# Optimization experiments

Hardware: AMD Instinct MI355X
Metric: run time of the kernel (lower is better)

Reference implementation:

```python
import jax, jax.numpy as jnp
import numpy as np

B, D, G, C = 4096, 512, 128, 10
THR = 0.95          # reliability_threshold
LR_MAX, LR_MIN = 0.2, 0.05
CTX_MAX, CTX_MIN = 2, 0


def setup_inputs() -> dict:
    key = jax.random.key(0)
    k1, k2, k3, k4, k5 = jax.random.split(key, 5)
    activations = jax.random.uniform(k1, (B, D), jnp.float32)
    labels = jax.random.randint(k2, (B,), 0, C)
    som_vectors = jax.random.uniform(k3, (G, G, D), jnp.float32) * 0.5 + 0.5
    cell_labels = jax.random.randint(k4, (G, G), 0, C)
    cell_reliability = jax.random.uniform(k5, (G, G), jnp.float32) * 100.0
    return dict(activations=activations, labels=labels, som_vectors=som_vectors,
                cell_labels=cell_labels, cell_reliability=cell_reliability,
                epoch=10, max_epochs=100)


def reference(activations, labels, som_vectors, cell_labels, cell_reliability, epoch, max_epochs):
    # --- schedule (static python scalars) ---
    progress = (max_epochs - epoch) / max_epochs if max_epochs > 0 else 0
    progress = max(0.0, min(1.0, progress))
    som_context = CTX_MIN + int(progress ** 4 * (CTX_MAX - CTX_MIN))
    som_lr = LR_MIN + progress * (LR_MAX - LR_MIN)

    flat_som = som_vectors.reshape(-1, D)                 # (N, D), N = G*G
    # --- squared-euclidean distance matrix (B, N) ---
    x_norm = jnp.sum(activations ** 2, axis=1, keepdims=True)
    w_norm = jnp.sum(flat_som ** 2, axis=1)[None, :]
    dists = jnp.clip(x_norm + w_norm - 2.0 * activations @ flat_som.T, 0.0, None)
    min_dists = jnp.min(dists, axis=1)
    bmu = jnp.argmin(dists, axis=1)                        # (B,)

    # --- class-constrained BMU for SOM error ---
    flat_labels = cell_labels.reshape(-1)
    label_mask = flat_labels[None, :] != labels[:, None]   # (B, N)
    class_dists = jnp.where(label_mask, jnp.inf, dists)
    class_bmu = jnp.argmin(class_dists, axis=1)
    class_bmu_vectors = flat_som[class_bmu]                # (B, D)
    rel = cell_reliability.reshape(-1)[class_bmu] / 100.0  # (B,)
    valid = (rel >= THR).astype(activations.dtype)
    som_errors = 0.01 * rel[:, None] * (class_bmu_vectors - activations) * valid[:, None]

    # --- batch neighborhood SOM update (matches torch code, incl. x/y convention) ---
    bmu_x = bmu // G
    bmu_y = bmu % G
    coords = jnp.arange(G)
    dist_y = jnp.abs(coords[None, :] - bmu_y[:, None])     # (B, G) rows (y_grid) vs bmu_y
    dist_x = jnp.abs(coords[None, :] - bmu_x[:, None])     # (B, G) cols (x_grid) vs bmu_x
    cheb = jnp.maximum(dist_y[:, :, None], dist_x[:, None, :])   # (B, G, G)
    powers = (som_lr / 2.0 ** cheb.astype(activations.dtype)) * (cheb <= som_context)
    denom = powers.sum(axis=0)[..., None]                  # (G, G, 1)
    numerator = jnp.einsum('bn,bd->nd', powers.reshape(B, -1), activations).reshape(G, G, D)
    updated = som_vectors + numerator - som_vectors * denom
    new_som = jnp.where(jnp.mean(min_dists) > 1e-4, updated, som_vectors)

    return som_errors, new_som
```

## Files before the change

### kernel.cpp

```cpp
#include <hip/hip_runtime.h>
#include <math.h>

#define B_ 4096
#define D_ 512
#define G_ 128
#define N_ (G_*G_)
#define NTP 64
#define THR_ 0.95f
#define IMAX_ 0x7FFFFFFF

typedef float f32x4 __attribute__((ext_vector_type(4)));
typedef _Float16 half8 __attribute__((ext_vector_type(8)));

__global__ __launch_bounds__(256) void prep_kernel(
    const float* __restrict__ A, const float* __restrict__ W,
    _Float16* __restrict__ Ahi, _Float16* __restrict__ Whi,
    float* __restrict__ wnorm, float* __restrict__ S,
    float* __restrict__ count, float* __restrict__ sum_min)
{
    const int blk = blockIdx.x, tid = threadIdx.x;
    if (blk < 2048) {
        int i = blk * 256 + tid;
        float4 v = ((const float4*)A)[i];
        float vv[4] = {v.x, v.y, v.z, v.w};
        union { _Float16 h[4]; uint64_t u64; } H;
        #pragma unroll
        for (int j = 0; j < 4; j++) H.h[j] = (_Float16)vv[j];
        ((uint64_t*)Ahi)[i] = H.u64;
    } else if (blk < 6144) {
        int n = (blk - 2048) * 4 + (tid >> 6);
        int t = tid & 63;
        const float* row = W + (size_t)n * D_;
        float4 a = ((const float4*)row)[t];
        float4 b = ((const float4*)row)[t + 64];
        float av[4] = {a.x, a.y, a.z, a.w}, bv[4] = {b.x, b.y, b.z, b.w};
        union { _Float16 h[4]; uint64_t u64; } Ha, Hb;
        #pragma unroll
        for (int j = 0; j < 4; j++) { Ha.h[j] = (_Float16)av[j]; Hb.h[j] = (_Float16)bv[j]; }
        ((uint64_t*)(Whi + (size_t)n * D_))[t]       = Ha.u64;
        ((uint64_t*)(Whi + (size_t)n * D_ + 256))[t] = Hb.u64;
        float s = a.x*a.x + a.y*a.y + a.z*a.z + a.w*a.w
                + b.x*b.x + b.y*b.y + b.z*b.z + b.w*b.w;
        #pragma unroll
        for (int off = 32; off > 0; off >>= 1) s += __shfl_down(s, off, 64);
        if (t == 0) wnorm[n] = s;
    } else if (blk < 6160) {
        if (blk == 6144 && tid < 65) sum_min[tid] = 0.f;
        int j = (blk - 6144) * 256 + tid;
        float4 z = {0.f, 0.f, 0.f, 0.f};
        ((float4*)count)[j] = z;
    } else {
        size_t i = (size_t)(blk - 6160) * 256 + tid;
        float4 z = {0.f, 0.f, 0.f, 0.f};
        ((float4*)S)[i] = z;
    }
}

__device__ __forceinline__ unsigned long long packmin(float v, int n) {
    unsigned u = __float_as_uint(v);
    u ^= (u & 0x80000000u) ? 0xFFFFFFFFu : 0x80000000u;
    return ((unsigned long long)u << 32) | (unsigned)n;
}
__device__ __forceinline__ void unpackmin(unsigned long long pkt, float* v, int* n) {
    unsigned u = (unsigned)(pkt >> 32);
    u = (u & 0x80000000u) ? (u ^ 0x80000000u) : ~u;
    *v = __uint_as_float(u);
    *n = (int)(unsigned)pkt;
}


#define PH_WAIT_(N) asm volatile("s_waitcnt vmcnt(" #N ")" ::: "memory")
#define PH_WAIT(N) PH_WAIT_(N)
#define WAITLGKM0 asm volatile("s_waitcnt lgkmcnt(0)" ::: "memory")
#define SBAR __builtin_amdgcn_s_barrier()
#define SCHED0 __builtin_amdgcn_sched_barrier(0)
#define PRIO1 __builtin_amdgcn_s_setprio(1)
#define PRIO0 __builtin_amdgcn_s_setprio(0)

#define STAGE_HALF(GBASE, LOFF, TAU, H) do { \
    __builtin_amdgcn_global_load_lds( \
        (const __attribute__((address_space(1))) void*)((GBASE) + (size_t)(H) * (128 * D_) + (TAU) * 64 + srcoff0), \
        (__attribute__((address_space(3))) void*)(smem + (LOFF) + (((TAU) & 1) << 15) + ((H) << 14) + ldsoff0), 16, 0, 0); \
    __builtin_amdgcn_global_load_lds( \
        (const __attribute__((address_space(1))) void*)((GBASE) + (size_t)(H) * (128 * D_) + (TAU) * 64 + srcoff1), \
        (__attribute__((address_space(3))) void*)(smem + (LOFF) + (((TAU) & 1) << 15) + ((H) << 14) + ldsoff1), 16, 0, 0); \
} while (0)

#define TILE(TAU, S1, S3, S4, DO_W, VM4) do { \
    half8 af[4][2], bl[2][2], bh[2][2]; \
    _Pragma("unroll") for (int mi = 0; mi < 4; mi++) { \
        af[mi][0] = *(const half8*)(smem + (((TAU) & 1) << 15) + sA + mi * 2048 + swz0); \
        af[mi][1] = *(const half8*)(smem + (((TAU) & 1) << 15) + sA + mi * 2048 + swz1); } \
    _Pragma("unroll") for (int ni = 0; ni < 2; ni++) { \
        bl[ni][0] = *(const half8*)(smem + 65536 + (((TAU) & 1) << 15) + sB + ni * 2048 + swz0); \
        bl[ni][1] = *(const half8*)(smem + 65536 + (((TAU) & 1) << 15) + sB + ni * 2048 + swz1); } \
    if (S1) STAGE_HALF(Abase, 0, (TAU) + 1, 1); \
    SBAR; WAITLGKM0; SCHED0; PRIO1; \
    _Pragma("unroll") for (int mi = 0; mi < 4; mi++) \
      _Pragma("unroll") for (int ni = 0; ni < 2; ni++) { \
        acc[mi][ni] = __builtin_amdgcn_mfma_f32_16x16x32_f16(af[mi][0], bl[ni][0], acc[mi][ni], 0, 0, 0); \
        acc[mi][ni] = __builtin_amdgcn_mfma_f32_16x16x32_f16(af[mi][1], bl[ni][1], acc[mi][ni], 0, 0, 0); } \
    PRIO0; SCHED0; SBAR; \
    _Pragma("unroll") for (int ni = 0; ni < 2; ni++) { \
        bh[ni][0] = *(const half8*)(smem + 65536 + (((TAU) & 1) << 15) + sB + (ni + 2) * 2048 + swz0); \
        bh[ni][1] = *(const half8*)(smem + 65536 + (((TAU) & 1) << 15) + sB + (ni + 2) * 2048 + swz1); } \
    SBAR; WAITLGKM0; SCHED0; PRIO1; \
    _Pragma("unroll") for (int mi = 0; mi < 4; mi++) \
      _Pragma("unroll") for (int ni = 0; ni < 2; ni++) { \
        acc[mi][ni + 2] = __builtin_amdgcn_mfma_f32_16x16x32_f16(af[mi][0], bh[ni][0], acc[mi][ni + 2], 0, 0, 0); \
        acc[mi][ni + 2] = __builtin_amdgcn_mfma_f32_16x16x32_f16(af[mi][1], bh[ni][1], acc[mi][ni + 2], 0, 0, 0); } \
    PRIO0; SCHED0; SBAR; \
    _Pragma("unroll") for (int mi = 0; mi < 4; mi++) { \
        af[mi][0] = *(const half8*)(smem + (((TAU) & 1) << 15) + sA + (mi + 4) * 2048 + swz0); \
        af[mi][1] = *(const half8*)(smem + (((TAU) & 1) << 15) + sA + (mi + 4) * 2048 + swz1); } \
    if (S3) STAGE_HALF(Wbase, 65536, (TAU) + 2, 0); \
    SBAR; WAITLGKM0; SCHED0; PRIO1; \
    _Pragma("unroll") for (int mi = 0; mi < 4; mi++) \
      _Pragma("unroll") for (int ni = 0; ni < 2; ni++) { \
        acc[mi + 4][ni + 2] = __builtin_amdgcn_mfma_f32_16x16x32_f16(af[mi][0], bh[ni][0], acc[mi + 4][ni + 2], 0, 0, 0); \
        acc[mi + 4][ni + 2] = __builtin_amdgcn_mfma_f32_16x16x32_f16(af[mi][1], bh[ni][1], acc[mi + 4][ni + 2], 0, 0, 0); } \
    PRIO0; SCHED0; SBAR; \
    if (S4) { STAGE_HALF(Abase, 0, (TAU) + 2, 0); STAGE_HALF(Wbase, 65536, (TAU) + 2, 1); } \
    if (DO_W) PH_WAIT(VM4); \
    SBAR; PRIO1; \
    _Pragma("unroll") for (int mi = 0; mi < 4; mi++) \
      _Pragma("unroll") for (int ni = 0; ni < 2; ni++) { \
        acc[mi + 4][ni] = __builtin_amdgcn_mfma_f32_16x16x32_f16(af[mi][0], bl[ni][0], acc[mi + 4][ni], 0, 0, 0); \
        acc[mi + 4][ni] = __builtin_amdgcn_mfma_f32_16x16x32_f16(af[mi][1], bl[ni][1], acc[mi + 4][ni], 0, 0, 0); } \
    PRIO0; SCHED0; SBAR; \
} while (0)

__global__ __launch_bounds__(512, 2) void score_mfma_kernel(
    const _Float16* __restrict__ Ah, const _Float16* __restrict__ Wh,
    const float* __restrict__ wnorm,
    const int* __restrict__ labels, const int* __restrict__ clabels,
    float* __restrict__ pminv, int* __restrict__ pmini,
    float* __restrict__ pcminv, int* __restrict__ pcmini)
{
    __shared__ __align__(16) char smem[131072];

    const int tid  = threadIdx.x;
    const int lane = tid & 63;
    const int wave = tid >> 6;
    const int wm = wave >> 2, wn = wave & 3;
    const int c = lane & 15, quad = lane >> 4;

    const int o = blockIdx.x;
    const int xcd = o & 7, idx = o >> 3;
    const int ntile = (xcd << 3) | (idx & 7);
    const int mtile = idx >> 3;
    const int m0 = mtile * 256, n0 = ntile * 256;

    const _Float16* Abase = Ah + (size_t)m0 * D_;
    const _Float16* Wbase = Wh + (size_t)n0 * D_;

    const int i0 = tid, i1 = 512 + tid;
    const int rl0 = i0 >> 3, sl0 = i0 & 7, rl1 = i1 >> 3, sl1 = i1 & 7;
    const size_t srcoff0 = (size_t)rl0 * D_ + ((sl0 ^ (rl0 & 7)) << 3);
    const size_t srcoff1 = (size_t)rl1 * D_ + ((sl1 ^ (rl1 & 7)) << 3);
    const int ldsoff0 = i0 << 4, ldsoff1 = i1 << 4;

    const int sA = (wm * 128 + c) * 128;
    const int sB = (wn * 64 + c) * 128;
    const int swz0 = ((0 * 4 + quad) ^ (c & 7)) << 4;
    const int swz1 = ((1 * 4 + quad) ^ (c & 7)) << 4;

    f32x4 acc[8][4];
    #pragma unroll
    for (int i = 0; i < 8; i++)
        #pragma unroll
        for (int j = 0; j < 4; j++)
            acc[i][j] = (f32x4){0.f, 0.f, 0.f, 0.f};

    STAGE_HALF(Abase, 0, 0, 0);
    STAGE_HALF(Wbase, 65536, 0, 0);
    STAGE_HALF(Wbase, 65536, 0, 1);
    STAGE_HALF(Abase, 0, 0, 1);
    STAGE_HALF(Abase, 0, 1, 0);
    STAGE_HALF(Wbase, 65536, 1, 0);
    STAGE_HALF(Wbase, 65536, 1, 1);
    PH_WAIT(6); SBAR;

    TILE(0, 1, 1, 1, 1, 6);
    TILE(1, 1, 1, 1, 1, 6);
    TILE(2, 1, 1, 1, 1, 6);
    TILE(3, 1, 1, 1, 1, 6);
    TILE(4, 1, 1, 1, 1, 6);
    TILE(5, 1, 1, 1, 1, 6);
    TILE(6, 1, 0, 0, 1, 0);
    TILE(7, 0, 0, 0, 0, 0);

    __syncthreads();

    const unsigned long long ID = (0xFF800000ull << 32) | 0x7FFFFFFFull;
    float wnl[4]; int cll[4];
    #pragma unroll
    for (int ni = 0; ni < 4; ni++) {
        int n = n0 + wn * 64 + ni * 16 + c;
        wnl[ni] = wnorm[n];
        cll[ni] = clabels[n];
    }

    unsigned long long (*tbl)[64] = (unsigned long long (*)[64])smem;
    unsigned long long cbst[8][4];

    #pragma unroll
    for (int mi = 0; mi < 8; mi++) {
        #pragma unroll
        for (int r = 0; r < 4; r++) {
            int rowl = wm * 128 + mi * 16 + quad * 4 + r;
            int lb = labels[m0 + rowl];
            unsigned long long bb = ID, cb = ID;
            #pragma unroll
            for (int ni = 0; ni < 4; ni++) {
                float s = fmaf(-2.f, acc[mi][ni][r], wnl[ni]);
                unsigned long long pk = packmin(s, n0 + wn * 64 + ni * 16 + c);
                bb = bb < pk ? bb : pk;
                if (cll[ni] == lb) cb = cb < pk ? cb : pk;
            }
            tbl[rowl][(wn * 16 + c) ^ (rowl & 15)] = bb;
            cbst[mi][r] = cb;
        }
    }
    __syncthreads();
    if (tid < 256) {
        int row = tid;
        unsigned long long m = ID;
        #pragma unroll
        for (int j = 0; j < 64; j++) {
            unsigned long long v = tbl[row][j ^ (row & 15)];
            m = m < v ? m : v;
        }
        float v; int n; unpackmin(m, &v, &n);
        size_t pp = (size_t)(m0 + row) * NTP + ntile;
        pminv[pp] = v; pmini[pp] = n;
    }
    __syncthreads();
    #pragma unroll
    for (int mi = 0; mi < 8; mi++)
        #pragma unroll
        for (int r = 0; r < 4; r++) {
            int rowl = wm * 128 + mi * 16 + quad * 4 + r;
            tbl[rowl][(wn * 16 + c) ^ (rowl & 15)] = cbst[mi][r];
        }
    __syncthreads();
    if (tid < 256) {
        int row = tid;
        unsigned long long m = ID;
        #pragma unroll
        for (int j = 0; j < 64; j++) {
            unsigned long long v = tbl[row][j ^ (row & 15)];
            m = m < v ? m : v;
        }
        float v; int n; unpackmin(m, &v, &n);
        size_t pp = (size_t)(m0 + row) * NTP + ntile;
        pcminv[pp] = v; pcmini[pp] = n;
    }
}

__global__ __launch_bounds__(256) void reduce_kernel(
    const float* __restrict__ A, const float* __restrict__ W,
    const float* __restrict__ crel,
    const float* __restrict__ pminv, const int* __restrict__ pmini,
    const float* __restrict__ pcminv, const int* __restrict__ pcmini,
    int* __restrict__ bmu, float* __restrict__ sum_min, float* __restrict__ out0,
    float* __restrict__ S, float* __restrict__ count)
{
    __shared__ int sbn[4];
    const int b = blockIdx.x * 4 + (threadIdx.x >> 6);
    const int l = threadIdx.x & 63;

    size_t p = (size_t)b * NTP + l;
    unsigned long long bb = packmin(pminv[p], pmini[p]);
    unsigned long long cb = packmin(pcminv[p], pcmini[p]);

    const float* arow = A + (size_t)b * D_;
    float4 xa = ((const float4*)arow)[l];
    float4 xb = ((const float4*)arow)[l + 64];
    float xs = xa.x*xa.x + xa.y*xa.y + xa.z*xa.z + xa.w*xa.w
             + xb.x*xb.x + xb.y*xb.y + xb.z*xb.z + xb.w*xb.w;

    #pragma unroll
    for (int off = 1; off < 64; off <<= 1) {
        unsigned long long ob = __shfl_xor(bb, off, 64);
        bb = bb < ob ? bb : ob;
        unsigned long long oc = __shfl_xor(cb, off, 64);
        cb = cb < oc ? cb : oc;
        xs += __shfl_xor(xs, off, 64);
    }

    float bv; int bn; unpackmin(bb, &bv, &bn);
    float cv; int cn; unpackmin(cb, &cv, &cn);

    if (l == 0) {
        bmu[b] = bn;
        sbn[threadIdx.x >> 6] = bn;
        float md = xs + bv;
        if (md < 0.f) md = 0.f;
        atomicAdd(&sum_min[b & 63], md);
        atomicAdd(&count[bn], 1.0f);
    }

    float r = crel[cn] / 100.0f;
    float sc = (r >= THR_) ? 0.01f * r : 0.f;
    const float* wrow = W + (size_t)cn * D_;
    float4 wa = ((const float4*)wrow)[l];
    float4 wb = ((const float4*)wrow)[l + 64];
    float4 oa, ob4;
    oa.x = sc * (wa.x - xa.x); oa.y = sc * (wa.y - xa.y);
    oa.z = sc * (wa.z - xa.z); oa.w = sc * (wa.w - xa.w);
    ob4.x = sc * (wb.x - xb.x); ob4.y = sc * (wb.y - xb.y);
    ob4.z = sc * (wb.z - xb.z); ob4.w = sc * (wb.w - xb.w);
    float* orow = out0 + (size_t)b * D_;
    ((float4*)orow)[l]      = oa;
    ((float4*)orow)[l + 64] = ob4;

    __syncthreads();
    const int base_b = blockIdx.x * 4;
    #pragma unroll
    for (int rr = 0; rr < 4; rr++) {
        int bm = sbn[rr];
        const float* ar = A + (size_t)(base_b + rr) * D_;
        float* Sr = S + (size_t)bm * D_;
        atomicAdd(&Sr[threadIdx.x],       ar[threadIdx.x]);
        atomicAdd(&Sr[threadIdx.x + 256], ar[threadIdx.x + 256]);
    }
}

__global__ __launch_bounds__(256) void final_kernel(
    const float* __restrict__ som, const float* __restrict__ S,
    const float* __restrict__ count, const float* __restrict__ sum_min,
    const int* __restrict__ epoch_p, const int* __restrict__ maxep_p,
    float* __restrict__ out1)
{
    __shared__ float gsum;
    if (threadIdx.x == 0) {
        float s = 0.f;
        for (int i = 0; i < 64; i++) s += sum_min[i];
        gsum = s;
    }
    __syncthreads();

    const int o = blockIdx.x;
    const int vb = ((o & 7) << 10) | (o >> 3);
    size_t i4 = (size_t)vb * 256 + threadIdx.x;
    int n = (int)(i4 >> 7);
    int d4 = (int)(i4 & 127);
    float4 s = ((const float4*)som)[i4];
    bool gate = gsum > 1e-4f * (float)B_;
    float4 ov = s;
    if (gate) {
        int ep = epoch_p[0], me = maxep_p[0];
        float progress = (me > 0) ? (float)(me - ep) / (float)me : 0.f;
        progress = fminf(fmaxf(progress, 0.f), 1.f);
        float p2 = progress * progress;
        int ctx = (int)(p2 * p2 * 2.0f);
        float lr = 0.05f + progress * 0.15f;

        int i = n / G_, j = n % G_;
        float4 nu = {0.f, 0.f, 0.f, 0.f};
        float dn = 0.f;
        for (int di = -ctx; di <= ctx; di++) {
            int ia = i - di; if (ia < 0 || ia >= G_) continue;
            for (int dj = -ctx; dj <= ctx; dj++) {
                int jb = j - dj; if (jb < 0 || jb >= G_) continue;
                int ad = abs(di), aj = abs(dj);
                int cheb = ad > aj ? ad : aj;
                float coef = ldexpf(lr, -cheb);
                float4 t4 = ((const float4*)S)[(size_t)(jb * G_ + ia) * 128 + d4];
                nu.x += coef * t4.x; nu.y += coef * t4.y;
                nu.z += coef * t4.z; nu.w += coef * t4.w;
                dn += coef * count[jb * G_ + ia];
            }
        }
        ov.x = s.x + nu.x - s.x * dn;
        ov.y = s.y + nu.y - s.y * dn;
        ov.z = s.z + nu.z - s.z * dn;
        ov.w = s.w + nu.w - s.w * dn;
    }
    ((float4*)out1)[i4] = ov;
}

extern "C" void kernel_launch(void* const* d_in, const int* in_sizes, int n_in,
                              void* d_out, int out_size, void* d_ws, size_t ws_size,
                              hipStream_t stream) {
    const float* A   = (const float*)d_in[0];
    const int*   lab = (const int*)d_in[1];
    const float* W   = (const float*)d_in[2];
    const int*   cl  = (const int*)d_in[3];
    const float* cr  = (const float*)d_in[4];
    const int*   ep  = (const int*)d_in[5];
    const int*   me  = (const int*)d_in[6];

    float* out0 = (float*)d_out;
    float* out1 = out0 + (size_t)B_ * D_;

    const size_t MB = 1024 * 1024;
    uint8_t* w = (uint8_t*)d_ws;
    _Float16* Ahi  = (_Float16*)(w);
    _Float16* Whi  = (_Float16*)(w + 4 * MB);
    float* pminv   = (float*)(w + 32 * MB);
    int*   pmini   = (int*)  (w + 34 * MB);
    float* pcminv  = (float*)(w + 36 * MB);
    int*   pcmini  = (int*)  (w + 38 * MB);
    float* wnorm   = (float*)(w + 40 * MB);
    float* count   = (float*)(w + 40 * MB + 128 * 1024);
    int*   bmu     = (int*)  (w + 40 * MB + 192 * 1024);
    float* sum_min = (float*)(w + 40 * MB + 256 * 1024);

    const int fused = (ws_size >= 80 * MB) ? 1 : 0;
    float* S = fused ? (float*)(w + 48 * MB) : (float*)w;

    prep_kernel<<<fused ? 14352 : 6160, 256, 0, stream>>>(
        A, W, Ahi, Whi, wnorm, S, count, sum_min);

    score_mfma_kernel<<<dim3((B_ / 256) * (N_ / 256)), 512, 0, stream>>>(
        Ahi, Whi, wnorm, lab, cl, pminv, pmini, pcminv, pcmini);

    if (!fused)
        hipMemsetAsync(S, 0, (size_t)N_ * D_ * sizeof(float), stream);

    reduce_kernel<<<B_ / 4, 256, 0, stream>>>(A, W, cr, pminv, pmini, pcminv, pcmini,
                                              bmu, sum_min, out0, S, count);

    final_kernel<<<(N_ * D_ / 4) / 256, 256, 0, stream>>>(
        W, S, count, sum_min, ep, me, out1);
}
```

Measured before the change: 258.1 us.

## Restructure MFMA k-tile pipeline to load all fragments once and stage per tile

Replaces the four-phase per-k-tile schedule, which interleaved partial LDS fragment loads, staged global loads and many barriers, with a simpler schedule. Each tile now loads all A and B fragments up front, runs half the MFMAs, then issues all staging loads for tile+2 and waits before running the other half. The aim is fewer barriers and less LDS/MFMA serialisation. In exchange it holds more fragment registers live and overlaps less finely, which could hurt occupancy or latency hiding at 2 blocks per CU.

Measured after the change: 260.9 us. About the same (+1.1%).

```diff
diff --git a/kernel.cpp b/kernel.cpp
--- a/kernel.cpp
+++ b/kernel.cpp
@@ -86,48 +86,37 @@
         (__attribute__((address_space(3))) void*)(smem + (LOFF) + (((TAU) & 1) << 15) + ((H) << 14) + ldsoff1), 16, 0, 0); \
 } while (0)
 
-#define TILE(TAU, S1, S3, S4, DO_W, VM4) do { \
-    half8 af[4][2], bl[2][2], bh[2][2]; \
-    _Pragma("unroll") for (int mi = 0; mi < 4; mi++) { \
-        af[mi][0] = *(const half8*)(smem + (((TAU) & 1) << 15) + sA + mi * 2048 + swz0); \
-        af[mi][1] = *(const half8*)(smem + (((TAU) & 1) << 15) + sA + mi * 2048 + swz1); } \
-    _Pragma("unroll") for (int ni = 0; ni < 2; ni++) { \
-        bl[ni][0] = *(const half8*)(smem + 65536 + (((TAU) & 1) << 15) + sB + ni * 2048 + swz0); \
-        bl[ni][1] = *(const half8*)(smem + 65536 + (((TAU) & 1) << 15) + sB + ni * 2048 + swz1); } \
-    if (S1) STAGE_HALF(Abase, 0, (TAU) + 1, 1); \
-    SBAR; WAITLGKM0; SCHED0; PRIO1; \
+#define TILE9(TAU, DO_STAGE, VMN, LAST) do { \
+    const int bo_ = ((TAU) & 1) << 15; \
+    half8 af[8][2], bf[4][2]; \
+    _Pragma("unroll") for (int mi = 0; mi < 8; mi++) { \
+        af[mi][0] = *(const half8*)(smem + bo_ + sA + mi * 2048 + swz0); \
+        af[mi][1] = *(const half8*)(smem + bo_ + sA + mi * 2048 + swz1); } \
+    _Pragma("unroll") for (int ni = 0; ni < 4; ni++) { \
+        bf[ni][0] = *(const half8*)(smem + 65536 + bo_ + sB + ni * 2048 + swz0); \
+        bf[ni][1] = *(const half8*)(smem + 65536 + bo_ + sB + ni * 2048 + swz1); } \
+    PRIO1; \
     _Pragma("unroll") for (int mi = 0; mi < 4; mi++) \
-      _Pragma("unroll") for (int ni = 0; ni < 2; ni++) { \
-        acc[mi][ni] = __builtin_amdgcn_mfma_f32_16x16x32_f16(af[mi][0], bl[ni][0], acc[mi][ni], 0, 0, 0); \
-        acc[mi][ni] = __builtin_amdgcn_mfma_f32_16x16x32_f16(af[mi][1], bl[ni][1], acc[mi][ni], 0, 0, 0); } \
-    PRIO0; SCHED0; SBAR; \
-    _Pragma("unroll") for (int ni = 0; ni < 2; ni++) { \
-        bh[ni][0] = *(const half8*)(smem + 65536 + (((TAU) & 1) << 15) + sB + (ni + 2) * 2048 + swz0); \
-        bh[ni][1] = *(const half8*)(smem + 65536 + (((TAU) & 1) << 15) + sB + (ni + 2) * 2048 + swz1); } \
-    SBAR; WAITLGKM0; SCHED0; PRIO1; \
-    _Pragma("unroll") for (int mi = 0; mi < 4; mi++) \
-      _Pragma("unroll") for (int ni = 0; ni < 2; ni++) { \
-        acc[mi][ni + 2] = __builtin_amdgcn_mfma_f32_16x16x32_f16(af[mi][0], bh[ni][0], acc[mi][ni + 2], 0, 0, 0); \
-        acc[mi][ni + 2] = __builtin_amdgcn_mfma_f32_16x16x32_f16(af[mi][1], bh[ni][1], acc[mi][ni + 2], 0, 0, 0); } \
-    PRIO0; SCHED0; SBAR; \
-    _Pragma("unroll") for (int mi = 0; mi < 4; mi++) { \
-        af[mi][0] = *(const half8*)(smem + (((TAU) & 1) << 15) + sA + (mi + 4) * 2048 + swz0); \
-        af[mi][1] = *(const half8*)(smem + (((TAU) & 1) << 15) + sA + (mi + 4) * 2048 + swz1); } \
-    if (S3) STAGE_HALF(Wbase, 65536, (TAU) + 2, 0); \
-    SBAR; WAITLGKM0; SCHED0; PRIO1; \
-    _Pragma("unroll") for (int mi = 0; mi < 4; mi++) \
-      _Pragma("unroll") for (int ni = 0; ni < 2; ni++) { \
-        acc[mi + 4][ni + 2] = __builtin_amdgcn_mfma_f32_16x16x32_f16(af[mi][0], bh[ni][0], acc[mi + 4][ni + 2], 0, 0, 0); \
-        acc[mi + 4][ni + 2] = __builtin_amdgcn_mfma_f32_16x16x32_f16(af[mi][1], bh[ni][1], acc[mi + 4][ni + 2], 0, 0, 0); } \
-    PRIO0; SCHED0; SBAR; \
-    if (S4) { STAGE_HALF(Abase, 0, (TAU) + 2, 0); STAGE_HALF(Wbase, 65536, (TAU) + 2, 1); } \
-    if (DO_W) PH_WAIT(VM4); \
-    SBAR; PRIO1; \
-    _Pragma("unroll") for (int mi = 0; mi < 4; mi++) \
-      _Pragma("unroll") for (int ni = 0; ni < 2; ni++) { \
-        acc[mi + 4][ni] = __builtin_amdgcn_mfma_f32_16x16x32_f16(af[mi][0], bl[ni][0], acc[mi + 4][ni], 0, 0, 0); \
-        acc[mi + 4][ni] = __builtin_amdgcn_mfma_f32_16x16x32_f16(af[mi][1], bl[ni][1], acc[mi + 4][ni], 0, 0, 0); } \
-    PRIO0; SCHED0; SBAR; \
+      _Pragma("unroll") for (int ni = 0; ni < 4; ni++) { \
+        acc[mi][ni] = __builtin_amdgcn_mfma_f32_16x16x32_f16(af[mi][0], bf[ni][0], acc[mi][ni], 0, 0, 0); \
+        acc[mi][ni] = __builtin_amdgcn_mfma_f32_16x16x32_f16(af[mi][1], bf[ni][1], acc[mi][ni], 0, 0, 0); } \
+    PRIO0; \
+    if (!(LAST)) { \
+        WAITLGKM0; SCHED0; SBAR; \
+        if (DO_STAGE) { \
+            STAGE_HALF(Abase, 0, (TAU) + 2, 0); \
+            STAGE_HALF(Abase, 0, (TAU) + 2, 1); \
+            STAGE_HALF(Wbase, 65536, (TAU) + 2, 0); \
+            STAGE_HALF(Wbase, 65536, (TAU) + 2, 1); \
+        } \
+        PH_WAIT(VMN); SBAR; \
+    } \
+    PRIO1; \
+    _Pragma("unroll") for (int mi = 4; mi < 8; mi++) \
+      _Pragma("unroll") for (int ni = 0; ni < 4; ni++) { \
+        acc[mi][ni] = __builtin_amdgcn_mfma_f32_16x16x32_f16(af[mi][0], bf[ni][0], acc[mi][ni], 0, 0, 0); \
+        acc[mi][ni] = __builtin_amdgcn_mfma_f32_16x16x32_f16(af[mi][1], bf[ni][1], acc[mi][ni], 0, 0, 0); } \
+    PRIO0; SCHED0; \
 } while (0)
 
 __global__ __launch_bounds__(512, 2) void score_mfma_kernel(
@@ -173,22 +162,23 @@
             acc[i][j] = (f32x4){0.f, 0.f, 0.f, 0.f};
 
     STAGE_HALF(Abase, 0, 0, 0);
+    STAGE_HALF(Abase, 0, 0, 1);
     STAGE_HALF(Wbase, 65536, 0, 0);
     STAGE_HALF(Wbase, 65536, 0, 1);
-    STAGE_HALF(Abase, 0, 0, 1);
     STAGE_HALF(Abase, 0, 1, 0);
+    STAGE_HALF(Abase, 0, 1, 1);
     STAGE_HALF(Wbase, 65536, 1, 0);
     STAGE_HALF(Wbase, 65536, 1, 1);
-    PH_WAIT(6); SBAR;
-
-    TILE(0, 1, 1, 1, 1, 6);
-    TILE(1, 1, 1, 1, 1, 6);
-    TILE(2, 1, 1, 1, 1, 6);
-    TILE(3, 1, 1, 1, 1, 6);
-    TILE(4, 1, 1, 1, 1, 6);
-    TILE(5, 1, 1, 1, 1, 6);
-    TILE(6, 1, 0, 0, 1, 0);
-    TILE(7, 0, 0, 0, 0, 0);
+    PH_WAIT(8); SBAR;
+
+    TILE9(0, 1, 8, 0);
+    TILE9(1, 1, 8, 0);
+    TILE9(2, 1, 8, 0);
+    TILE9(3, 1, 8, 0);
+    TILE9(4, 1, 8, 0);
+    TILE9(5, 1, 8, 0);
+    TILE9(6, 0, 0, 0);
+    TILE9(7, 0, 0, 1);
 
     __syncthreads();
 
```

## Fuse prep, score, reduce and update kernels into one cooperative persistent kernel

Applied to the files above, without the earlier changes.

Replaces the four-kernel pipeline with a single cooperative kernel of 256 blocks that runs the fp16 conversion, the MFMA score tiles, the BMU reduction and the SOM update as phases separated by grid-wide syncs. The goal is to remove kernel launch gaps and tail effects between stages. In exchange, the score phase now loops over 1024 tiles with only 256 resident blocks, and each phase is limited to the persistent grid's parallelism. Grid syncs add their own overhead, and the fallback path is kept for devices without cooperative launch.

Result: slower. 527.9 us (+104.5%).

```diff
diff --git a/kernel.cpp b/kernel.cpp
--- a/kernel.cpp
+++ b/kernel.cpp
@@ -1,5 +1,8 @@
 #include <hip/hip_runtime.h>
+#include <hip/hip_cooperative_groups.h>
 #include <math.h>
+
+namespace cg = cooperative_groups;
 
 #define B_ 4096
 #define D_ 512
@@ -11,50 +14,6 @@
 
 typedef float f32x4 __attribute__((ext_vector_type(4)));
 typedef _Float16 half8 __attribute__((ext_vector_type(8)));
-
-__global__ __launch_bounds__(256) void prep_kernel(
-    const float* __restrict__ A, const float* __restrict__ W,
-    _Float16* __restrict__ Ahi, _Float16* __restrict__ Whi,
-    float* __restrict__ wnorm, float* __restrict__ S,
-    float* __restrict__ count, float* __restrict__ sum_min)
-{
-    const int blk = blockIdx.x, tid = threadIdx.x;
-    if (blk < 2048) {
-        int i = blk * 256 + tid;
-        float4 v = ((const float4*)A)[i];
-        float vv[4] = {v.x, v.y, v.z, v.w};
-        union { _Float16 h[4]; uint64_t u64; } H;
-        #pragma unroll
-        for (int j = 0; j < 4; j++) H.h[j] = (_Float16)vv[j];
-        ((uint64_t*)Ahi)[i] = H.u64;
-    } else if (blk < 6144) {
-        int n = (blk - 2048) * 4 + (tid >> 6);
-        int t = tid & 63;
-        const float* row = W + (size_t)n * D_;
-        float4 a = ((const float4*)row)[t];
-        float4 b = ((const float4*)row)[t + 64];
-        float av[4] = {a.x, a.y, a.z, a.w}, bv[4] = {b.x, b.y, b.z, b.w};
-        union { _Float16 h[4]; uint64_t u64; } Ha, Hb;
-        #pragma unroll
-        for (int j = 0; j < 4; j++) { Ha.h[j] = (_Float16)av[j]; Hb.h[j] = (_Float16)bv[j]; }
-        ((uint64_t*)(Whi + (size_t)n * D_))[t]       = Ha.u64;
-        ((uint64_t*)(Whi + (size_t)n * D_ + 256))[t] = Hb.u64;
-        float s = a.x*a.x + a.y*a.y + a.z*a.z + a.w*a.w
-                + b.x*b.x + b.y*b.y + b.z*b.z + b.w*b.w;
-        #pragma unroll
-        for (int off = 32; off > 0; off >>= 1) s += __shfl_down(s, off, 64);
-        if (t == 0) wnorm[n] = s;
-    } else if (blk < 6160) {
-        if (blk == 6144 && tid < 65) sum_min[tid] = 0.f;
-        int j = (blk - 6144) * 256 + tid;
-        float4 z = {0.f, 0.f, 0.f, 0.f};
-        ((float4*)count)[j] = z;
-    } else {
-        size_t i = (size_t)(blk - 6160) * 256 + tid;
-        float4 z = {0.f, 0.f, 0.f, 0.f};
-        ((float4*)S)[i] = z;
-    }
-}
 
 __device__ __forceinline__ unsigned long long packmin(float v, int n) {
     unsigned u = __float_as_uint(v);
@@ -130,8 +89,8 @@
     PRIO0; SCHED0; SBAR; \
 } while (0)
 
-__global__ __launch_bounds__(512, 2) void score_mfma_kernel(
-    const _Float16* __restrict__ Ah, const _Float16* __restrict__ Wh,
+__device__ __forceinline__ void score_tile_body(
+    int o, const _Float16* __restrict__ Ah, const _Float16* __restrict__ Wh,
     const float* __restrict__ wnorm,
     const int* __restrict__ labels, const int* __restrict__ clabels,
     float* __restrict__ pminv, int* __restrict__ pmini,
@@ -145,7 +104,6 @@
     const int wm = wave >> 2, wn = wave & 3;
     const int c = lane & 15, quad = lane >> 4;
 
-    const int o = blockIdx.x;
     const int xcd = o & 7, idx = o >> 3;
     const int ntile = (xcd << 3) | (idx & 7);
     const int mtile = idx >> 3;
@@ -256,6 +214,247 @@
         size_t pp = (size_t)(m0 + row) * NTP + ntile;
         pcminv[pp] = v; pcmini[pp] = n;
     }
+    __syncthreads();
+}
+
+__global__ __launch_bounds__(512, 2) void mega_kernel(
+    const float* __restrict__ A, const int* __restrict__ labels,
+    const float* __restrict__ W, const int* __restrict__ clabels,
+    const float* __restrict__ crel,
+    const int* __restrict__ epoch_p, const int* __restrict__ maxep_p,
+    _Float16* __restrict__ Ahi, _Float16* __restrict__ Whi,
+    float* __restrict__ wnorm,
+    float* __restrict__ pminv, int* __restrict__ pmini,
+    float* __restrict__ pcminv, int* __restrict__ pcmini,
+    int* __restrict__ bmu, float* __restrict__ sum_min,
+    float* __restrict__ out0, float* __restrict__ out1,
+    float* __restrict__ S, float* __restrict__ count, int fusedS)
+{
+    cg::grid_group grid = cg::this_grid();
+    const int tid  = threadIdx.x;
+    const int blk  = blockIdx.x;
+    const int gtid = blk * 512 + tid;
+    const int GS   = 256 * 512;
+
+    {
+        const float4 z = {0.f, 0.f, 0.f, 0.f};
+        #pragma unroll
+        for (int it = 0; it < 4; it++) {
+            int i = gtid + it * GS;
+            float4 v = ((const float4*)A)[i];
+            float vv[4] = {v.x, v.y, v.z, v.w};
+            union { _Float16 h[4]; uint64_t u64; } H;
+            #pragma unroll
+            for (int j = 0; j < 4; j++) H.h[j] = (_Float16)vv[j];
+            ((uint64_t*)Ahi)[i] = H.u64;
+        }
+        const int t = tid & 63;
+        #pragma unroll
+        for (int it = 0; it < 8; it++) {
+            int n = (gtid >> 6) + it * (GS >> 6);
+            const float* row = W + (size_t)n * D_;
+            float4 a = ((const float4*)row)[t];
+            float4 bq = ((const float4*)row)[t + 64];
+            float av[4] = {a.x, a.y, a.z, a.w}, bv[4] = {bq.x, bq.y, bq.z, bq.w};
+            union { _Float16 h[4]; uint64_t u64; } Ha, Hb;
+            #pragma unroll
+            for (int j = 0; j < 4; j++) { Ha.h[j] = (_Float16)av[j]; Hb.h[j] = (_Float16)bv[j]; }
+            ((uint64_t*)(Whi + (size_t)n * D_))[t]       = Ha.u64;
+            ((uint64_t*)(Whi + (size_t)n * D_ + 256))[t] = Hb.u64;
+            float s = a.x*a.x + a.y*a.y + a.z*a.z + a.w*a.w
+                    + bq.x*bq.x + bq.y*bq.y + bq.z*bq.z + bq.w*bq.w;
+            #pragma unroll
+            for (int off = 32; off > 0; off >>= 1) s += __shfl_down(s, off, 64);
+            if (t == 0) wnorm[n] = s;
+        }
+        if (gtid < N_ / 4) ((float4*)count)[gtid] = z;
+        if (gtid < 65) sum_min[gtid] = 0.f;
+        if (fusedS) {
+            #pragma unroll
+            for (int it = 0; it < 16; it++)
+                ((float4*)S)[(size_t)gtid + (size_t)it * GS] = z;
+        }
+    }
+    __threadfence();
+    grid.sync();
+
+    for (int o = blk; o < 1024; o += 256)
+        score_tile_body(o, Ahi, Whi, wnorm, labels, clabels,
+                        pminv, pmini, pcminv, pcmini);
+    __threadfence();
+    grid.sync();
+
+    if (!fusedS) {
+        const float4 z = {0.f, 0.f, 0.f, 0.f};
+        #pragma unroll
+        for (int it = 0; it < 16; it++)
+            ((float4*)S)[(size_t)gtid + (size_t)it * GS] = z;
+        __threadfence();
+        grid.sync();
+    }
+
+    {
+        const int l = tid & 63;
+        #pragma unroll
+        for (int it = 0; it < 2; it++) {
+            int rw = (gtid >> 6) + it * (GS >> 6);
+            size_t p = (size_t)rw * NTP + l;
+            unsigned long long bb = packmin(pminv[p], pmini[p]);
+            unsigned long long cb = packmin(pcminv[p], pcmini[p]);
+
+            const float* arow = A + (size_t)rw * D_;
+            float4 xa = ((const float4*)arow)[l];
+            float4 xb = ((const float4*)arow)[l + 64];
+            float xs = xa.x*xa.x + xa.y*xa.y + xa.z*xa.z + xa.w*xa.w
+                     + xb.x*xb.x + xb.y*xb.y + xb.z*xb.z + xb.w*xb.w;
+
+            #pragma unroll
+            for (int off = 1; off < 64; off <<= 1) {
+                unsigned long long ob = __shfl_xor(bb, off, 64);
+                bb = bb < ob ? bb : ob;
+                unsigned long long oc = __shfl_xor(cb, off, 64);
+                cb = cb < oc ? cb : oc;
+                xs += __shfl_xor(xs, off, 64);
+            }
+
+            float bv; int bn; unpackmin(bb, &bv, &bn);
+            float cv; int cn; unpackmin(cb, &cv, &cn);
+
+            if (l == 0) {
+                bmu[rw] = bn;
+                float md = xs + bv;
+                if (md < 0.f) md = 0.f;
+                atomicAdd(&sum_min[rw & 63], md);
+                atomicAdd(&count[bn], 1.0f);
+            }
+
+            float rel = crel[cn] / 100.0f;
+            float sc = (rel >= THR_) ? 0.01f * rel : 0.f;
+            const float* wrow = W + (size_t)cn * D_;
+            float4 wa = ((const float4*)wrow)[l];
+            float4 wb = ((const float4*)wrow)[l + 64];
+            float4 oa, ob4;
+            oa.x = sc * (wa.x - xa.x); oa.y = sc * (wa.y - xa.y);
+            oa.z = sc * (wa.z - xa.z); oa.w = sc * (wa.w - xa.w);
+            ob4.x = sc * (wb.x - xb.x); ob4.y = sc * (wb.y - xb.y);
+            ob4.z = sc * (wb.z - xb.z); ob4.w = sc * (wb.w - xb.w);
+            float* orow = out0 + (size_t)rw * D_;
+            ((float4*)orow)[l]      = oa;
+            ((float4*)orow)[l + 64] = ob4;
+
+            float* Sr = S + (size_t)bn * D_;
+            #pragma unroll
+            for (int k = 0; k < 8; k++)
+                atomicAdd(&Sr[k * 64 + l], arow[k * 64 + l]);
+        }
+    }
+    __threadfence();
+    grid.sync();
+
+    {
+        __shared__ float gsum_s;
+        if (tid == 0) {
+            float s = 0.f;
+            for (int i = 0; i < 64; i++) s += sum_min[i];
+            gsum_s = s;
+        }
+        __syncthreads();
+        const bool gate = gsum_s > 1e-4f * (float)B_;
+
+        int ep = epoch_p[0], me = maxep_p[0];
+        float progress = (me > 0) ? (float)(me - ep) / (float)me : 0.f;
+        progress = fminf(fmaxf(progress, 0.f), 1.f);
+        float p2 = progress * progress;
+        int ctx = (int)(p2 * p2 * 2.0f);
+        float lr = 0.05f + progress * 0.15f;
+
+        const int x = blk & 7, wsub = blk >> 3;
+        for (int it = 0; it < 16; it++) {
+            size_t i4 = (size_t)x * 262144 + (size_t)it * 16384 + (size_t)wsub * 512 + tid;
+            int n = (int)(i4 >> 7);
+            int d4 = (int)(i4 & 127);
+            float4 s4 = ((const float4*)W)[i4];
+            float4 ov = s4;
+            if (gate) {
+                int i = n / G_, j = n % G_;
+                float4 nu = {0.f, 0.f, 0.f, 0.f};
+                float dn = 0.f;
+                for (int di = -ctx; di <= ctx; di++) {
+                    int ia = i - di; if (ia < 0 || ia >= G_) continue;
+                    for (int dj = -ctx; dj <= ctx; dj++) {
+                        int jb = j - dj; if (jb < 0 || jb >= G_) continue;
+                        int ad = abs(di), aj = abs(dj);
+                        int cheb = ad > aj ? ad : aj;
+                        float coef = ldexpf(lr, -cheb);
+                        float4 t4 = ((const float4*)S)[(size_t)(jb * G_ + ia) * 128 + d4];
+                        nu.x += coef * t4.x; nu.y += coef * t4.y;
+                        nu.z += coef * t4.z; nu.w += coef * t4.w;
+                        dn += coef * count[jb * G_ + ia];
+                    }
+                }
+                ov.x = s4.x + nu.x - s4.x * dn;
+                ov.y = s4.y + nu.y - s4.y * dn;
+                ov.z = s4.z + nu.z - s4.z * dn;
+                ov.w = s4.w + nu.w - s4.w * dn;
+            }
+            ((float4*)out1)[i4] = ov;
+        }
+    }
+}
+
+__global__ __launch_bounds__(256) void prep_kernel(
+    const float* __restrict__ A, const float* __restrict__ W,
+    _Float16* __restrict__ Ahi, _Float16* __restrict__ Whi,
+    float* __restrict__ wnorm, float* __restrict__ S,
+    float* __restrict__ count, float* __restrict__ sum_min)
+{
+    const int blk = blockIdx.x, tid = threadIdx.x;
+    if (blk < 2048) {
+        int i = blk * 256 + tid;
+        float4 v = ((const float4*)A)[i];
+        float vv[4] = {v.x, v.y, v.z, v.w};
+        union { _Float16 h[4]; uint64_t u64; } H;
+        #pragma unroll
+        for (int j = 0; j < 4; j++) H.h[j] = (_Float16)vv[j];
+        ((uint64_t*)Ahi)[i] = H.u64;
+    } else if (blk < 6144) {
+        int n = (blk - 2048) * 4 + (tid >> 6);
+        int t = tid & 63;
+        const float* row = W + (size_t)n * D_;
+        float4 a = ((const float4*)row)[t];
+        float4 b = ((const float4*)row)[t + 64];
+        float av[4] = {a.x, a.y, a.z, a.w}, bv[4] = {b.x, b.y, b.z, b.w};
+        union { _Float16 h[4]; uint64_t u64; } Ha, Hb;
+        #pragma unroll
+        for (int j = 0; j < 4; j++) { Ha.h[j] = (_Float16)av[j]; Hb.h[j] = (_Float16)bv[j]; }
+        ((uint64_t*)(Whi + (size_t)n * D_))[t]       = Ha.u64;
+        ((uint64_t*)(Whi + (size_t)n * D_ + 256))[t] = Hb.u64;
+        float s = a.x*a.x + a.y*a.y + a.z*a.z + a.w*a.w
+                + b.x*b.x + b.y*b.y + b.z*b.z + b.w*b.w;
+        #pragma unroll
+        for (int off = 32; off > 0; off >>= 1) s += __shfl_down(s, off, 64);
+        if (t == 0) wnorm[n] = s;
+    } else if (blk < 6160) {
+        if (blk == 6144 && tid < 65) sum_min[tid] = 0.f;
+        int j = (blk - 6144) * 256 + tid;
+        float4 z = {0.f, 0.f, 0.f, 0.f};
+        ((float4*)count)[j] = z;
+    } else {
+        size_t i = (size_t)(blk - 6160) * 256 + tid;
+        float4 z = {0.f, 0.f, 0.f, 0.f};
+        ((float4*)S)[i] = z;
+    }
+}
+
+__global__ __launch_bounds__(512, 2) void score_mfma_kernel(
+    const _Float16* __restrict__ Ah, const _Float16* __restrict__ Wh,
+    const float* __restrict__ wnorm,
+    const int* __restrict__ labels, const int* __restrict__ clabels,
+    float* __restrict__ pminv, int* __restrict__ pmini,
+    float* __restrict__ pcminv, int* __restrict__ pcmini)
+{
+    score_tile_body(blockIdx.x, Ah, Wh, wnorm, labels, clabels,
+                    pminv, pmini, pcminv, pcmini);
 }
 
 __global__ __launch_bounds__(256) void reduce_kernel(
@@ -408,21 +607,44 @@
     int*   bmu     = (int*)  (w + 40 * MB + 192 * 1024);
     float* sum_min = (float*)(w + 40 * MB + 256 * 1024);
 
-    const int fused = (ws_size >= 80 * MB) ? 1 : 0;
-    float* S = fused ? (float*)(w + 48 * MB) : (float*)w;
-
-    prep_kernel<<<fused ? 14352 : 6160, 256, 0, stream>>>(
-        A, W, Ahi, Whi, wnorm, S, count, sum_min);
-
-    score_mfma_kernel<<<dim3((B_ / 256) * (N_ / 256)), 512, 0, stream>>>(
-        Ahi, Whi, wnorm, lab, cl, pminv, pmini, pcminv, pcmini);
-
-    if (!fused)
-        hipMemsetAsync(S, 0, (size_t)N_ * D_ * sizeof(float), stream);
-
-    reduce_kernel<<<B_ / 4, 256, 0, stream>>>(A, W, cr, pminv, pmini, pcminv, pcmini,
-                                              bmu, sum_min, out0, S, count);
-
-    final_kernel<<<(N_ * D_ / 4) / 256, 256, 0, stream>>>(
-        W, S, count, sum_min, ep, me, out1);
-}
+    const int fusedS = (ws_size >= 80 * MB) ? 1 : 0;
+    float* S = fusedS ? (float*)(w + 48 * MB) : (float*)w;
+
+    static int coop = -1;
+    if (coop < 0) {
+        int dev = 0;
+        (void)hipGetDevice(&dev);
+        int v = 0;
+        if (hipDeviceGetAttribute(&v, hipDeviceAttributeCooperativeLaunch, dev) != hipSuccess)
+            v = 0;
+        coop = v;
+    }
+
+    if (coop) {
+        int fusedS_arg = fusedS;
+        void* kargs[] = {
+            (void*)&A, (void*)&lab, (void*)&W, (void*)&cl, (void*)&cr,
+            (void*)&ep, (void*)&me, (void*)&Ahi, (void*)&Whi, (void*)&wnorm,
+            (void*)&pminv, (void*)&pmini, (void*)&pcminv, (void*)&pcmini,
+            (void*)&bmu, (void*)&sum_min, (void*)&out0, (void*)&out1,
+            (void*)&S, (void*)&count, (void*)&fusedS_arg
+        };
+        hipLaunchCooperativeKernel((const void*)mega_kernel, dim3(256), dim3(512),
+                                   kargs, 0, stream);
+    } else {
+        prep_kernel<<<fusedS ? 14352 : 6160, 256, 0, stream>>>(
+            A, W, Ahi, Whi, wnorm, S, count, sum_min);
+
+        score_mfma_kernel<<<dim3((B_ / 256) * (N_ / 256)), 512, 0, stream>>>(
+            Ahi, Whi, wnorm, lab, cl, pminv, pmini, pcminv, pcmini);
+
+        if (!fusedS)
+            hipMemsetAsync(S, 0, (size_t)N_ * D_ * sizeof(float), stream);
+
+        reduce_kernel<<<B_ / 4, 256, 0, stream>>>(A, W, cr, pminv, pmini, pcminv, pcmini,
+                                                  bmu, sum_min, out0, S, count);
+
+        final_kernel<<<(N_ * D_ / 4) / 256, 256, 0, stream>>>(
+            W, S, count, sum_min, ep, me, out1);
+    }
+}
```
